# Kernel optimization log

Measured on AMD Instinct MI355X. Metric: run time of the kernel, lower is better.

Reference implementation:

```python
import jax, jax.numpy as jnp
import numpy as np

REF_CHANNEL = 0
DIAG_EPS = 1e-7   # diag_loading coefficient
TIK_EPS = 1e-8    # additive eps in diagonal loading / trace denominator
MASK_EPS = 1e-15  # PSD mask-normalization eps


def _psd(spec, mask):
    # spec: (b, c, f, t) complex; mask: (b, f, t) real
    # PSD module: normalize mask over time, weight outer products, sum over t.
    m = mask / (mask.sum(axis=-1, keepdims=True) + MASK_EPS)
    return jnp.einsum('bcft,beft,bft->bfce', spec, spec.conj(), m.astype(spec.dtype))


def setup_inputs() -> dict:
    key = jax.random.key(0)
    k1, k2, k3, k4 = jax.random.split(key, 4)
    B, C, F, T = 4, 6, 257, 2000
    return {
        'spec_real': jax.random.normal(k1, (B, C, F, T), dtype=jnp.float32),
        'spec_imag': jax.random.normal(k2, (B, C, F, T), dtype=jnp.float32),
        'mask_s': jax.random.uniform(k3, (B, F, T), dtype=jnp.float32),
        'mask_n': jax.random.uniform(k4, (B, F, T), dtype=jnp.float32),
    }


def reference(spec_real, spec_imag, mask_s, mask_n):
    spec = spec_real + 1j * spec_imag                     # (b, c, f, t) complex64
    C = spec.shape[1]

    psd_s = _psd(spec, mask_s)                            # (b, f, c, c)
    psd_n = _psd(spec, mask_n)                            # (b, f, c, c)

    # Diagonal loading (Tikhonov regularization) of the noise PSD.
    tr_n = jnp.einsum('bfcc->bf', psd_n).real
    epsilon = jax.lax.stop_gradient(tr_n * DIAG_EPS + TIK_EPS)   # torch uses no_grad here
    psd_n = psd_n + epsilon[..., None, None] * jnp.eye(C, dtype=spec.dtype)

    # ref_channel solution: w = (psd_n^-1 psd_s) / trace(psd_n^-1 psd_s) @ u
    numerator = jnp.linalg.solve(psd_n, psd_s)            # (b, f, c, c)
    tr = jnp.einsum('bfcc->bf', numerator)
    ws = numerator / (tr[..., None, None] + TIK_EPS)
    w = ws[..., :, REF_CHANNEL]                           # one-hot u selects column -> (b, f, c)

    # enhanced = w^H Y
    enh = jnp.einsum('bfc,bcft->bft', w.conj(), spec)     # (b, f, t) complex
    return jnp.stack([enh.real, enh.imag], axis=-1)       # (b, f, t, 2) float32
```

## Files before the change

kernel.cpp:

```cpp
#include <hip/hip_runtime.h>

#define NB 4
#define NC 6
#define NF 257
#define NT 2000
#define NG (NB * NF)
#define NPAIR 15
#define NACC 74
#define NCHUNK 4
#define TCH (NT / NCHUNK)
#define NP2 (TCH / 2)
#define BLK 256
#define CS  (NF * NT)
#define CS2 (CS / 2)

typedef float nfloat4 __attribute__((ext_vector_type(4)));

template<int CTRL>
__device__ __forceinline__ float dpp_add(float v) {
    int s = __builtin_amdgcn_update_dpp(0, __builtin_bit_cast(int, v), CTRL, 0xF, 0xF, true);
    return v + __builtin_bit_cast(float, s);
}

__global__ __launch_bounds__(BLK) void psd_kernel(
    const float* __restrict__ sr, const float* __restrict__ si,
    const float* __restrict__ ms, const float* __restrict__ mn,
    float* __restrict__ wsp)
{
    constexpr int PC[NPAIR] = {0,0,0,0,0,1,1,1,1,2,2,2,3,3,4};
    constexpr int PE[NPAIR] = {1,2,3,4,5,2,3,4,5,3,4,5,4,5,5};

    const int bx = blockIdx.x;
    const int g  = bx >> 2;
    const int b  = g / NF;
    const int f  = g - b * NF;
    const int tb = (bx & 3) * TCH;
    const int sbase = b * NC * CS + f * NT + tb;
    const int mbase = g * NT + tb;

    const float2* s2r = (const float2*)(sr + sbase);
    const float2* s2i = (const float2*)(si + sbase);
    const float2* m2s = (const float2*)(ms + mbase);
    const float2* m2n = (const float2*)(mn + mbase);

    float acc[NACC];
    #pragma unroll
    for (int i = 0; i < NACC; i++) acc[i] = 0.f;

    const bool act = threadIdx.x < NP2;
    const int  p   = act ? threadIdx.x : 0;
    {
        float wms[2], wmn[2], rr[NC][2], ii[NC][2];
        {
            const float2 t0 = m2s[p];
            wms[0] = t0.x; wms[1] = t0.y;
            const float2 t1 = m2n[p];
            wmn[0] = t1.x; wmn[1] = t1.y;
        }
        #pragma unroll
        for (int c = 0; c < NC; c++) {
            const float2 tr = s2r[c * CS2 + p];
            rr[c][0] = tr.x; rr[c][1] = tr.y;
            const float2 ti = s2i[c * CS2 + p];
            ii[c][0] = ti.x; ii[c][1] = ti.y;
        }
        if (!act) { wms[0] = wms[1] = wmn[0] = wmn[1] = 0.f; }
        #pragma unroll
        for (int k = 0; k < 2; k++) { acc[72] += wms[k]; acc[73] += wmn[k]; }
        #pragma unroll
        for (int c = 0; c < NC; c++) {
            #pragma unroll
            for (int k = 0; k < 2; k++) {
                const float d = rr[c][k] * rr[c][k] + ii[c][k] * ii[c][k];
                acc[c]     += d * wms[k];
                acc[6 + c] += d * wmn[k];
            }
        }
        #pragma unroll
        for (int q = 0; q < NPAIR; q++) {
            const int c = PC[q], e = PE[q];
            #pragma unroll
            for (int k = 0; k < 2; k++) {
                const float cr = rr[c][k] * rr[e][k] + ii[c][k] * ii[e][k];
                const float ci = ii[c][k] * rr[e][k] - rr[c][k] * ii[e][k];
                acc[12 + 4 * q + 0] += cr * wms[k];
                acc[12 + 4 * q + 1] += ci * wms[k];
                acc[12 + 4 * q + 2] += cr * wmn[k];
                acc[12 + 4 * q + 3] += ci * wmn[k];
            }
        }
    }

    #pragma unroll
    for (int i = 0; i < NACC; i++) {
        float v = acc[i];
        v = dpp_add<0x118>(v);
        v = dpp_add<0x114>(v);
        v = dpp_add<0x112>(v);
        acc[i] = v;
    }

    __shared__ float red[32][NACC];
    const int lane16 = threadIdx.x & 15;
    const int ridx   = ((threadIdx.x >> 4) << 1) | (lane16 & 1);
    if (lane16 >= 14) {
        #pragma unroll
        for (int i = 0; i < NACC; i++) red[ridx][i] = acc[i];
    }
    __syncthreads();

    if (threadIdx.x < NACC) {
        float s = 0.f;
        #pragma unroll
        for (int r = 0; r < 32; r++) s += red[r][threadIdx.x];
        wsp[bx * NACC + threadIdx.x] = s;
    }
}

__global__ __launch_bounds__(64, 1) void solve_kernel(
    const float* __restrict__ wsp, float* __restrict__ wsw)
{
    const int gid = blockIdx.x * 64 + threadIdx.x;
    if (gid >= NG) return;

    constexpr int PC[NPAIR] = {0,0,0,0,0,1,1,1,1,2,2,2,3,3,4};
    constexpr int PE[NPAIR] = {1,2,3,4,5,2,3,4,5,3,4,5,4,5,5};
    constexpr int QIDX[NC][NC] = {
        {-1, 0, 1, 2, 3, 4},
        {-1,-1, 5, 6, 7, 8},
        {-1,-1,-1, 9,10,11},
        {-1,-1,-1,-1,12,13},
        {-1,-1,-1,-1,-1,14},
        {-1,-1,-1,-1,-1,-1}};

    const float* p0 = wsp + (NCHUNK * gid) * NACC;
    float fin[NACC];
    #pragma unroll
    for (int i = 0; i < NACC; i++)
        fin[i] = (p0[i] + p0[NACC + i]) + (p0[2 * NACC + i] + p0[3 * NACC + i]);

    const float invS = 1.f / (fin[72] + 1e-15f);
    const float invN = 1.f / (fin[73] + 1e-15f);

    float Ar[NC][NC], Ai[NC][NC];
    #pragma unroll
    for (int c = 0; c < NC; c++) { Ar[c][c] = fin[6 + c] * invN; Ai[c][c] = 0.f; }
    #pragma unroll
    for (int q = 0; q < NPAIR; q++) {
        const int c = PC[q], e = PE[q];
        const float nre = fin[12 + 4 * q + 2] * invN;
        const float nim = fin[12 + 4 * q + 3] * invN;
        Ar[c][e] = nre;  Ai[c][e] = nim;
        Ar[e][c] = nre;  Ai[e][c] = -nim;
    }
    {
        float trn = 0.f;
        #pragma unroll
        for (int c = 0; c < NC; c++) trn += Ar[c][c];
        const float eps = trn * 1e-7f + 1e-8f;
        #pragma unroll
        for (int c = 0; c < NC; c++) Ar[c][c] += eps;
    }

    #pragma unroll
    for (int k = 0; k < NC; k++) {
        const float dr = Ar[k][k], di = Ai[k][k];
        const float idn = 1.f / (dr * dr + di * di);
        const float pr = dr * idn, pi = -di * idn;
        #pragma unroll
        for (int i = k + 1; i < NC; i++) {
            const float lr = Ar[i][k] * pr - Ai[i][k] * pi;
            const float li = Ar[i][k] * pi + Ai[i][k] * pr;
            Ar[i][k] = lr; Ai[i][k] = li;
            #pragma unroll
            for (int j = k + 1; j < NC; j++) {
                Ar[i][j] -= lr * Ar[k][j] - li * Ai[k][j];
                Ai[i][j] -= lr * Ai[k][j] + li * Ar[k][j];
            }
        }
    }

    float trr = 1e-8f, tri = 0.f;
    float w0r[NC], w0i[NC];
    #pragma unroll
    for (int j = 0; j < NC; j++) {
        float xr[NC], xi[NC];
        #pragma unroll
        for (int i = 0; i < NC; i++) {
            if (i == j)      { xr[i] = fin[j] * invS;                      xi[i] = 0.f; }
            else if (i < j)  { const int q = QIDX[i][j];
                               xr[i] = fin[12 + 4 * q] * invS;  xi[i] =  fin[13 + 4 * q] * invS; }
            else             { const int q = QIDX[j][i];
                               xr[i] = fin[12 + 4 * q] * invS;  xi[i] = -fin[13 + 4 * q] * invS; }
        }
        #pragma unroll
        for (int i = 1; i < NC; i++) {
            #pragma unroll
            for (int k = 0; k < NC - 1; k++) if (k < i) {
                xr[i] -= Ar[i][k] * xr[k] - Ai[i][k] * xi[k];
                xi[i] -= Ar[i][k] * xi[k] + Ai[i][k] * xr[k];
            }
        }
        #pragma unroll
        for (int i = NC - 1; i >= 0; i--) {
            #pragma unroll
            for (int k = 0; k < NC; k++) if (k > i) {
                xr[i] -= Ar[i][k] * xr[k] - Ai[i][k] * xi[k];
                xi[i] -= Ar[i][k] * xi[k] + Ai[i][k] * xr[k];
            }
            const float dr = Ar[i][i], di = Ai[i][i];
            const float idn = 1.f / (dr * dr + di * di);
            const float pr = dr * idn, pi = -di * idn;
            const float tr0 = xr[i] * pr - xi[i] * pi;
            xi[i] = xr[i] * pi + xi[i] * pr;
            xr[i] = tr0;
        }
        trr += xr[j]; tri += xi[j];
        if (j == 0) {
            #pragma unroll
            for (int i = 0; i < NC; i++) { w0r[i] = xr[i]; w0i[i] = xi[i]; }
        }
    }

    const float idn = 1.f / (trr * trr + tri * tri);
    #pragma unroll
    for (int c = 0; c < NC; c++) {
        const float wre = (w0r[c] * trr + w0i[c] * tri) * idn;
        const float wim = (w0i[c] * trr - w0r[c] * tri) * idn;
        wsw[gid * 12 + c]     = wre;
        wsw[gid * 12 + 6 + c] = -wim;
    }
}

__global__ __launch_bounds__(BLK) void apply_kernel(
    const float* __restrict__ sr, const float* __restrict__ si,
    const float* __restrict__ wsw, float* __restrict__ out)
{
    const int bx = blockIdx.x;
    const int g  = bx >> 2;
    const int b  = g / NF;
    const int f  = g - b * NF;
    const int tb = (bx & 3) * TCH;
    const int sbase = b * NC * CS + f * NT + tb;

    const float2* s2r = (const float2*)(sr + sbase);
    const float2* s2i = (const float2*)(si + sbase);

    float wr[NC], wi[NC];
    #pragma unroll
    for (int c = 0; c < NC; c++) {
        wr[c] = wsw[g * 12 + c];
        wi[c] = wsw[g * 12 + 6 + c];
    }

    nfloat4* o4 = (nfloat4*)(out + 2 * (g * NT + tb));

    const int p = threadIdx.x;
    if (p < NP2) {
        float rr[NC][2], ii[NC][2];
        #pragma unroll
        for (int c = 0; c < NC; c++) {
            const float2 tr = s2r[c * CS2 + p];
            rr[c][0] = tr.x; rr[c][1] = tr.y;
            const float2 ti = s2i[c * CS2 + p];
            ii[c][0] = ti.x; ii[c][1] = ti.y;
        }
        float er[2], ei[2];
        #pragma unroll
        for (int k = 0; k < 2; k++) {
            float a = 0.f, bb = 0.f;
            #pragma unroll
            for (int c = 0; c < NC; c++) {
                a  += wr[c] * rr[c][k] - wi[c] * ii[c][k];
                bb += wr[c] * ii[c][k] + wi[c] * rr[c][k];
            }
            er[k] = a; ei[k] = bb;
        }
        nfloat4 o0 = {er[0], ei[0], er[1], ei[1]};
        __builtin_nontemporal_store(o0, &o4[p]);
    }
}

extern "C" void kernel_launch(void* const* d_in, const int* in_sizes, int n_in,
                              void* d_out, int out_size, void* d_ws, size_t ws_size,
                              hipStream_t stream) {
    const float* sr = (const float*)d_in[0];
    const float* si = (const float*)d_in[1];
    const float* ms = (const float*)d_in[2];
    const float* mn = (const float*)d_in[3];
    float* out = (float*)d_out;

    float* wsp = (float*)d_ws;
    float* wsw = wsp + NG * NCHUNK * NACC;

    psd_kernel<<<NG * NCHUNK, BLK, 0, stream>>>(sr, si, ms, mn, wsp);
    solve_kernel<<<(NG + 63) / 64, 64, 0, stream>>>(wsp, wsw);
    apply_kernel<<<NG * NCHUNK, BLK, 0, stream>>>(sr, si, wsw, out);
}
```

Before: 163.1 us.

## Fuse PSD, solve and apply into one kernel per frequency bin

Merges the three kernels into a single kernel with one block per (batch, frequency) group, each thread covering four time chunks. Per-chunk PSD partials no longer round-trip through global memory, and two launch boundaries disappear. The 6x6 solve is split across six threads, one per right-hand-side column, and the weights pass through shared memory so the apply step can re-read the spectrum while it may still be in cache. In exchange the grid shrinks to 1028 blocks, and the serial solve inside each block leaves the other threads idle.

```diff
diff --git a/kernel.cpp b/kernel.cpp
--- a/kernel.cpp
+++ b/kernel.cpp
@@ -7,10 +7,9 @@
 #define NG (NB * NF)
 #define NPAIR 15
 #define NACC 74
-#define NCHUNK 4
-#define TCH (NT / NCHUNK)
-#define NP2 (TCH / 2)
 #define BLK 256
+#define NP2 (NT / 2)
+#define NJ 4
 #define CS  (NF * NT)
 #define CS2 (CS / 2)
 
@@ -22,21 +21,24 @@
     return v + __builtin_bit_cast(float, s);
 }
 
-__global__ __launch_bounds__(BLK) void psd_kernel(
+__device__ __forceinline__ int qidx(int c, int e) {
+    return c * (2 * NC - 1 - c) / 2 + (e - c - 1);
+}
+
+__global__ __launch_bounds__(BLK) void mvdr_fused(
     const float* __restrict__ sr, const float* __restrict__ si,
     const float* __restrict__ ms, const float* __restrict__ mn,
-    float* __restrict__ wsp)
+    float* __restrict__ out)
 {
     constexpr int PC[NPAIR] = {0,0,0,0,0,1,1,1,1,2,2,2,3,3,4};
     constexpr int PE[NPAIR] = {1,2,3,4,5,2,3,4,5,3,4,5,4,5,5};
 
-    const int bx = blockIdx.x;
-    const int g  = bx >> 2;
+    const int g  = blockIdx.x;
     const int b  = g / NF;
     const int f  = g - b * NF;
-    const int tb = (bx & 3) * TCH;
-    const int sbase = b * NC * CS + f * NT + tb;
-    const int mbase = g * NT + tb;
+    const int sbase = b * NC * CS + f * NT;
+    const int mbase = g * NT;
+    const int tid = threadIdx.x;
 
     const float2* s2r = (const float2*)(sr + sbase);
     const float2* s2i = (const float2*)(si + sbase);
@@ -47,9 +49,11 @@
     #pragma unroll
     for (int i = 0; i < NACC; i++) acc[i] = 0.f;
 
-    const bool act = threadIdx.x < NP2;
-    const int  p   = act ? threadIdx.x : 0;
-    {
+    #pragma unroll
+    for (int j = 0; j < NJ; j++) {
+        const int q0 = j * BLK + tid;
+        const bool act = q0 < NP2;
+        const int p = act ? q0 : 0;
         float wms[2], wmn[2], rr[NC][2], ii[NC][2];
         {
             const float2 t0 = m2s[p];
@@ -101,97 +105,76 @@
     }
 
     __shared__ float red[32][NACC];
-    const int lane16 = threadIdx.x & 15;
-    const int ridx   = ((threadIdx.x >> 4) << 1) | (lane16 & 1);
+    __shared__ float fin[NACC];
+    __shared__ float sdr[NC], sdi[NC];
+    __shared__ float wsh[2 * NC];
+
+    const int lane16 = tid & 15;
+    const int ridx   = ((tid >> 4) << 1) | (lane16 & 1);
     if (lane16 >= 14) {
         #pragma unroll
         for (int i = 0; i < NACC; i++) red[ridx][i] = acc[i];
     }
     __syncthreads();
 
-    if (threadIdx.x < NACC) {
+    if (tid < NACC) {
         float s = 0.f;
         #pragma unroll
-        for (int r = 0; r < 32; r++) s += red[r][threadIdx.x];
-        wsp[bx * NACC + threadIdx.x] = s;
-    }
-}
-
-__global__ __launch_bounds__(64, 1) void solve_kernel(
-    const float* __restrict__ wsp, float* __restrict__ wsw)
-{
-    const int gid = blockIdx.x * 64 + threadIdx.x;
-    if (gid >= NG) return;
-
-    constexpr int PC[NPAIR] = {0,0,0,0,0,1,1,1,1,2,2,2,3,3,4};
-    constexpr int PE[NPAIR] = {1,2,3,4,5,2,3,4,5,3,4,5,4,5,5};
-    constexpr int QIDX[NC][NC] = {
-        {-1, 0, 1, 2, 3, 4},
-        {-1,-1, 5, 6, 7, 8},
-        {-1,-1,-1, 9,10,11},
-        {-1,-1,-1,-1,12,13},
-        {-1,-1,-1,-1,-1,14},
-        {-1,-1,-1,-1,-1,-1}};
-
-    const float* p0 = wsp + (NCHUNK * gid) * NACC;
-    float fin[NACC];
-    #pragma unroll
-    for (int i = 0; i < NACC; i++)
-        fin[i] = (p0[i] + p0[NACC + i]) + (p0[2 * NACC + i] + p0[3 * NACC + i]);
-
-    const float invS = 1.f / (fin[72] + 1e-15f);
-    const float invN = 1.f / (fin[73] + 1e-15f);
-
-    float Ar[NC][NC], Ai[NC][NC];
-    #pragma unroll
-    for (int c = 0; c < NC; c++) { Ar[c][c] = fin[6 + c] * invN; Ai[c][c] = 0.f; }
-    #pragma unroll
-    for (int q = 0; q < NPAIR; q++) {
-        const int c = PC[q], e = PE[q];
-        const float nre = fin[12 + 4 * q + 2] * invN;
-        const float nim = fin[12 + 4 * q + 3] * invN;
-        Ar[c][e] = nre;  Ai[c][e] = nim;
-        Ar[e][c] = nre;  Ai[e][c] = -nim;
-    }
-    {
-        float trn = 0.f;
-        #pragma unroll
-        for (int c = 0; c < NC; c++) trn += Ar[c][c];
-        const float eps = trn * 1e-7f + 1e-8f;
-        #pragma unroll
-        for (int c = 0; c < NC; c++) Ar[c][c] += eps;
-    }
-
-    #pragma unroll
-    for (int k = 0; k < NC; k++) {
-        const float dr = Ar[k][k], di = Ai[k][k];
-        const float idn = 1.f / (dr * dr + di * di);
-        const float pr = dr * idn, pi = -di * idn;
-        #pragma unroll
-        for (int i = k + 1; i < NC; i++) {
-            const float lr = Ar[i][k] * pr - Ai[i][k] * pi;
-            const float li = Ar[i][k] * pi + Ai[i][k] * pr;
-            Ar[i][k] = lr; Ai[i][k] = li;
-            #pragma unroll
-            for (int j = k + 1; j < NC; j++) {
-                Ar[i][j] -= lr * Ar[k][j] - li * Ai[k][j];
-                Ai[i][j] -= lr * Ai[k][j] + li * Ar[k][j];
-            }
-        }
-    }
-
-    float trr = 1e-8f, tri = 0.f;
-    float w0r[NC], w0i[NC];
-    #pragma unroll
-    for (int j = 0; j < NC; j++) {
-        float xr[NC], xi[NC];
+        for (int r = 0; r < 32; r++) s += red[r][tid];
+        fin[tid] = s;
+    }
+    __syncthreads();
+
+    float xr[NC], xi[NC];
+    if (tid < NC) {
+        const float invS = 1.f / (fin[72] + 1e-15f);
+        const float invN = 1.f / (fin[73] + 1e-15f);
+
+        float Ar[NC][NC], Ai[NC][NC];
+        #pragma unroll
+        for (int c = 0; c < NC; c++) { Ar[c][c] = fin[6 + c] * invN; Ai[c][c] = 0.f; }
+        #pragma unroll
+        for (int q = 0; q < NPAIR; q++) {
+            const int c = PC[q], e = PE[q];
+            const float nre = fin[12 + 4 * q + 2] * invN;
+            const float nim = fin[12 + 4 * q + 3] * invN;
+            Ar[c][e] = nre;  Ai[c][e] = nim;
+            Ar[e][c] = nre;  Ai[e][c] = -nim;
+        }
+        {
+            float trn = 0.f;
+            #pragma unroll
+            for (int c = 0; c < NC; c++) trn += Ar[c][c];
+            const float eps = trn * 1e-7f + 1e-8f;
+            #pragma unroll
+            for (int c = 0; c < NC; c++) Ar[c][c] += eps;
+        }
+
+        #pragma unroll
+        for (int k = 0; k < NC; k++) {
+            const float dr = Ar[k][k], di = Ai[k][k];
+            const float idn = 1.f / (dr * dr + di * di);
+            const float pr = dr * idn, pi = -di * idn;
+            #pragma unroll
+            for (int i = k + 1; i < NC; i++) {
+                const float lr = Ar[i][k] * pr - Ai[i][k] * pi;
+                const float li = Ar[i][k] * pi + Ai[i][k] * pr;
+                Ar[i][k] = lr; Ai[i][k] = li;
+                #pragma unroll
+                for (int j = k + 1; j < NC; j++) {
+                    Ar[i][j] -= lr * Ar[k][j] - li * Ai[k][j];
+                    Ai[i][j] -= lr * Ai[k][j] + li * Ar[k][j];
+                }
+            }
+        }
+
         #pragma unroll
         for (int i = 0; i < NC; i++) {
-            if (i == j)      { xr[i] = fin[j] * invS;                      xi[i] = 0.f; }
-            else if (i < j)  { const int q = QIDX[i][j];
-                               xr[i] = fin[12 + 4 * q] * invS;  xi[i] =  fin[13 + 4 * q] * invS; }
-            else             { const int q = QIDX[j][i];
-                               xr[i] = fin[12 + 4 * q] * invS;  xi[i] = -fin[13 + 4 * q] * invS; }
+            if (i == tid)      { xr[i] = fin[i] * invS;  xi[i] = 0.f; }
+            else if (i < tid)  { const int q = qidx(i, tid);
+                                 xr[i] = fin[12 + 4 * q] * invS;  xi[i] =  fin[13 + 4 * q] * invS; }
+            else               { const int q = qidx(tid, i);
+                                 xr[i] = fin[12 + 4 * q] * invS;  xi[i] = -fin[13 + 4 * q] * invS; }
         }
         #pragma unroll
         for (int i = 1; i < NC; i++) {
@@ -211,73 +194,63 @@
             const float dr = Ar[i][i], di = Ai[i][i];
             const float idn = 1.f / (dr * dr + di * di);
             const float pr = dr * idn, pi = -di * idn;
-            const float tr0 = xr[i] * pr - xi[i] * pi;
+            const float t0 = xr[i] * pr - xi[i] * pi;
             xi[i] = xr[i] * pi + xi[i] * pr;
-            xr[i] = tr0;
-        }
-        trr += xr[j]; tri += xi[j];
-        if (j == 0) {
-            #pragma unroll
-            for (int i = 0; i < NC; i++) { w0r[i] = xr[i]; w0i[i] = xi[i]; }
-        }
-    }
-
-    const float idn = 1.f / (trr * trr + tri * tri);
-    #pragma unroll
-    for (int c = 0; c < NC; c++) {
-        const float wre = (w0r[c] * trr + w0i[c] * tri) * idn;
-        const float wim = (w0i[c] * trr - w0r[c] * tri) * idn;
-        wsw[gid * 12 + c]     = wre;
-        wsw[gid * 12 + 6 + c] = -wim;
-    }
-}
-
-__global__ __launch_bounds__(BLK) void apply_kernel(
-    const float* __restrict__ sr, const float* __restrict__ si,
-    const float* __restrict__ wsw, float* __restrict__ out)
-{
-    const int bx = blockIdx.x;
-    const int g  = bx >> 2;
-    const int b  = g / NF;
-    const int f  = g - b * NF;
-    const int tb = (bx & 3) * TCH;
-    const int sbase = b * NC * CS + f * NT + tb;
-
-    const float2* s2r = (const float2*)(sr + sbase);
-    const float2* s2i = (const float2*)(si + sbase);
+            xr[i] = t0;
+        }
+        float dgr = xr[0], dgi = xi[0];
+        #pragma unroll
+        for (int i = 1; i < NC; i++) if (tid == i) { dgr = xr[i]; dgi = xi[i]; }
+        sdr[tid] = dgr; sdi[tid] = dgi;
+    }
+    __syncthreads();
+
+    if (tid == 0) {
+        float trr = 1e-8f, tri = 0.f;
+        #pragma unroll
+        for (int c = 0; c < NC; c++) { trr += sdr[c]; tri += sdi[c]; }
+        const float idn = 1.f / (trr * trr + tri * tri);
+        #pragma unroll
+        for (int c = 0; c < NC; c++) {
+            const float wre = (xr[c] * trr + xi[c] * tri) * idn;
+            const float wim = (xi[c] * trr - xr[c] * tri) * idn;
+            wsh[c]      = wre;
+            wsh[6 + c]  = -wim;
+        }
+    }
+    __syncthreads();
 
     float wr[NC], wi[NC];
     #pragma unroll
-    for (int c = 0; c < NC; c++) {
-        wr[c] = wsw[g * 12 + c];
-        wi[c] = wsw[g * 12 + 6 + c];
-    }
-
-    nfloat4* o4 = (nfloat4*)(out + 2 * (g * NT + tb));
-
-    const int p = threadIdx.x;
-    if (p < NP2) {
-        float rr[NC][2], ii[NC][2];
-        #pragma unroll
-        for (int c = 0; c < NC; c++) {
-            const float2 tr = s2r[c * CS2 + p];
-            rr[c][0] = tr.x; rr[c][1] = tr.y;
-            const float2 ti = s2i[c * CS2 + p];
-            ii[c][0] = ti.x; ii[c][1] = ti.y;
-        }
-        float er[2], ei[2];
-        #pragma unroll
-        for (int k = 0; k < 2; k++) {
-            float a = 0.f, bb = 0.f;
+    for (int c = 0; c < NC; c++) { wr[c] = wsh[c]; wi[c] = wsh[6 + c]; }
+
+    nfloat4* o4 = (nfloat4*)(out + 2 * mbase);
+    #pragma unroll
+    for (int j = 0; j < NJ; j++) {
+        const int p = j * BLK + tid;
+        if (p < NP2) {
+            float rr[NC][2], ii[NC][2];
             #pragma unroll
             for (int c = 0; c < NC; c++) {
-                a  += wr[c] * rr[c][k] - wi[c] * ii[c][k];
-                bb += wr[c] * ii[c][k] + wi[c] * rr[c][k];
-            }
-            er[k] = a; ei[k] = bb;
-        }
-        nfloat4 o0 = {er[0], ei[0], er[1], ei[1]};
-        __builtin_nontemporal_store(o0, &o4[p]);
+                const float2 tr = s2r[c * CS2 + p];
+                rr[c][0] = tr.x; rr[c][1] = tr.y;
+                const float2 ti = s2i[c * CS2 + p];
+                ii[c][0] = ti.x; ii[c][1] = ti.y;
+            }
+            float er[2], ei[2];
+            #pragma unroll
+            for (int k = 0; k < 2; k++) {
+                float a = 0.f, bb = 0.f;
+                #pragma unroll
+                for (int c = 0; c < NC; c++) {
+                    a  += wr[c] * rr[c][k] - wi[c] * ii[c][k];
+                    bb += wr[c] * ii[c][k] + wi[c] * rr[c][k];
+                }
+                er[k] = a; ei[k] = bb;
+            }
+            nfloat4 o0 = {er[0], ei[0], er[1], ei[1]};
+            __builtin_nontemporal_store(o0, &o4[p]);
+        }
     }
 }
 
@@ -289,11 +262,7 @@
     const float* ms = (const float*)d_in[2];
     const float* mn = (const float*)d_in[3];
     float* out = (float*)d_out;
-
-    float* wsp = (float*)d_ws;
-    float* wsw = wsp + NG * NCHUNK * NACC;
-
-    psd_kernel<<<NG * NCHUNK, BLK, 0, stream>>>(sr, si, ms, mn, wsp);
-    solve_kernel<<<(NG + 63) / 64, 64, 0, stream>>>(wsp, wsw);
-    apply_kernel<<<NG * NCHUNK, BLK, 0, stream>>>(sr, si, wsw, out);
-}
+    (void)d_ws; (void)ws_size;
+
+    mvdr_fused<<<NG, BLK, 0, stream>>>(sr, si, ms, mn, out);
+}
```

Result: slower. 176.7 us (+8.3%).
